# Optimization experiments

Hardware: AMD Instinct MI355X
Metric: run time of the kernel (lower is better)

The kernel has to match this reference:

```python
import jax, jax.numpy as jnp
import numpy as np

N0, P1 = 10000, 30000
N1 = N0 + P1            # 40000
P2 = 120000
N2 = N1 + P2            # 160000
E0, E1, E2 = 60000, 120000, 480000
IN, H, OUT, K = 3, 192, 3, 2


def setup_inputs() -> dict:
    key = jax.random.key(0)
    k = jax.random.split(key, 13)
    return {
        "features": jax.random.normal(k[0], (N0, IN), jnp.float32),
        "src0": jax.random.randint(k[1], (E0,), 0, N0, jnp.int32),
        "dst0": jax.random.randint(k[2], (E0,), 0, N0, jnp.int32),
        "pool_idx0": jax.random.randint(k[3], (P1, 2), 0, N0, jnp.int32),
        "edge0": jax.random.randint(k[4], (E1, 2), 0, N1, jnp.int32),
        "pool_idx1": jax.random.randint(k[5], (P2, 2), 0, N1, jnp.int32),
        "edge1": jax.random.randint(k[6], (E2, 2), 0, N2, jnp.int32),
        "W_first": 0.3 * jax.random.normal(k[7], (3, (K + 1) * IN, H), jnp.float32),
        "b_first": jnp.zeros((3, H), jnp.float32),
        "W_mid": 0.04 * jax.random.normal(k[8], (3, 12, (K + 1) * H, H), jnp.float32),
        "b_mid": jnp.zeros((3, 12, H), jnp.float32),
        "W_last": 0.05 * jax.random.normal(k[9], (3, (K + 1) * H, OUT), jnp.float32),
        "b_last": jnp.zeros((3, OUT), jnp.float32),
    }


def _norm(dst, n):
    # symmetric-norm factor D^{-1/2}, degrees clamped at 1 (DGL TAGConv)
    deg = jax.ops.segment_sum(jnp.ones(dst.shape[0], jnp.float32), dst, num_segments=n)
    return jnp.clip(deg, 1.0) ** -0.5  # [n]


def _tagconv(x, src, dst, n, norm, W, b):
    fs = [x]
    h = x
    for _ in range(K):
        h = norm[:, None] * jax.ops.segment_sum((h * norm[:, None])[src], dst, num_segments=n)
        fs.append(h)
    return jnp.concatenate(fs, axis=1) @ W + b


def _stage(x, src, dst, n, Wf, bf, Wm, bm, Wl, bl):
    norm = _norm(dst, n)
    h = jax.nn.relu(_tagconv(x, src, dst, n, norm, Wf, bf))
    prev = h  # raw output of previous layer (hidden[-2] in the torch code)
    for i in range(12):
        cur = jax.nn.relu(_tagconv(h, src, dst, n, norm, Wm[i], bm[i]))
        h = 0.5 * (prev + cur) if (i + 1) in (2, 4, 6, 8, 10, 12) else cur
        prev = cur
    return _tagconv(h, src, dst, n, norm, Wl, bl)  # identity activation


def _unpool(feat, pool_idx):
    # new vertex = midpoint of its two parents; appended to the node table
    new_vs = 0.5 * (feat[pool_idx[:, 0]] + feat[pool_idx[:, 1]])
    return jnp.concatenate([feat, new_vs], axis=0)


def _bidir(edge):
    # graph.add_edges(src, dst); graph.add_edges(dst, src)
    return (jnp.concatenate([edge[:, 0], edge[:, 1]]),
            jnp.concatenate([edge[:, 1], edge[:, 0]]))


def reference(features, src0, dst0, pool_idx0, edge0, pool_idx1, edge1,
              W_first, b_first, W_mid, b_mid, W_last, b_last):
    out1 = _stage(features, src0, dst0, N0,
                  W_first[0], b_first[0], W_mid[0], b_mid[0], W_last[0], b_last[0])
    h = _unpool(out1, pool_idx0)            # [N1, 3]
    out1_2 = h
    s1, d1 = _bidir(edge0)
    out2 = _stage(h, s1, d1, N1,
                  W_first[1], b_first[1], W_mid[1], b_mid[1], W_last[1], b_last[1])
    h = _unpool(out2, pool_idx1)            # [N2, 3]
    out2_2 = h
    s2, d2 = _bidir(edge1)
    out3 = _stage(h, s2, d2, N2,
                  W_first[2], b_first[2], W_mid[2], b_mid[2], W_last[2], b_last[2])
    return (out1, out2, out3, out1_2, out2_2)
```

## Files before the change

### kernel.cpp

```cpp
#include <hip/hip_runtime.h>
#include <hip/hip_fp16.h>

#define HF 192

static inline int divup(int a, int b){ return (a+b-1)/b; }

typedef _Float16 half8 __attribute__((ext_vector_type(8)));
typedef float f32x4 __attribute__((ext_vector_type(4)));

#define G_WS_BYTES 195734272ull
__device__ __align__(256) char g_ws[G_WS_BYTES];

#define OFF_HH    0ull
#define OFF_T1H   61440000ull
#define OFF_T2H   122880000ull
#define OFF_DEG  184320000ull
#define OFF_RP   184960000ull
#define OFF_COL  185600032ull
#define OFF_NRM  189440032ull
#define OFF_O1F  190080032ull
#define OFF_U1F  190200032ull
#define OFF_O2F  190680032ull
#define OFF_U2F  191160032ull
#define OFF_WT   193080032ull
#define OFF_X1F  OFF_T1H
#define OFF_X2F  (OFF_T1H + 1920000ull)

__device__ __forceinline__ float*  wsf(unsigned long long o){ return (float*) (g_ws + o); }
__device__ __forceinline__ int*    wsi(unsigned long long o){ return (int*)   (g_ws + o); }
__device__ __forceinline__ __half* wsh(unsigned long long o){ return (__half*)(g_ws + o); }

__global__ void k_zero(unsigned long long off, int n) {
  int i = blockIdx.x*blockDim.x + threadIdx.x;
  if (i < n) wsi(off)[i] = 0;
}
__global__ void k_copyi(unsigned long long aOff, unsigned long long bOff, int n) {
  int i = blockIdx.x*blockDim.x + threadIdx.x;
  if (i < n) wsi(bOff)[i] = wsi(aOff)[i];
}

__global__ void k_count_direct(const int* __restrict__ dst, int E) {
  int* deg = wsi(OFF_DEG);
  int e = blockIdx.x*blockDim.x + threadIdx.x;
  if (e < E) atomicAdd(&deg[dst[e]], 1);
}
__global__ void k_count_bidir(const int* __restrict__ edge, int E) {
  int* deg = wsi(OFF_DEG);
  int e = blockIdx.x*blockDim.x + threadIdx.x;
  if (e < E) {
    atomicAdd(&deg[edge[2*e+1]], 1);
    atomicAdd(&deg[edge[2*e  ]], 1);
  }
}
__global__ void k_norm(int n) {
  const int* deg = wsi(OFF_DEG);
  float* nrm = wsf(OFF_NRM);
  int i = blockIdx.x*blockDim.x + threadIdx.x;
  if (i < n) {
    int d = deg[i]; if (d < 1) d = 1;
    nrm[i] = rsqrtf((float)d);
  }
}
__global__ __launch_bounds__(1024) void k_exscan(int n) {
  const int* in = wsi(OFF_DEG);
  int* out = wsi(OFF_RP);
  __shared__ int sm[1024];
  int t = threadIdx.x;
  int carry = 0;
  for (int base = 0; base < n; base += 4096) {
    int idx = base + t*4;
    int v0 = (idx+0 < n) ? in[idx+0] : 0;
    int v1 = (idx+1 < n) ? in[idx+1] : 0;
    int v2 = (idx+2 < n) ? in[idx+2] : 0;
    int v3 = (idx+3 < n) ? in[idx+3] : 0;
    int s = v0+v1+v2+v3;
    sm[t] = s;
    __syncthreads();
    for (int off = 1; off < 1024; off <<= 1) {
      int u = (t >= off) ? sm[t-off] : 0;
      __syncthreads();
      sm[t] += u;
      __syncthreads();
    }
    int excl = carry + sm[t] - s;
    if (idx   < n) out[idx]   = excl;
    if (idx+1 < n) out[idx+1] = excl + v0;
    if (idx+2 < n) out[idx+2] = excl + v0+v1;
    if (idx+3 < n) out[idx+3] = excl + v0+v1+v2;
    carry += sm[1023];
    __syncthreads();
  }
  if (t == 0) out[n] = carry;
}
__global__ void k_fill_direct(const int* __restrict__ src, const int* __restrict__ dst, int E) {
  int* cur = wsi(OFF_DEG);
  int* col = wsi(OFF_COL);
  int e = blockIdx.x*blockDim.x + threadIdx.x;
  if (e < E) {
    int p = atomicAdd(&cur[dst[e]], 1);
    col[p] = src[e];
  }
}
__global__ void k_fill_bidir(const int* __restrict__ edge, int E) {
  int* cur = wsi(OFF_DEG);
  int* col = wsi(OFF_COL);
  int e = blockIdx.x*blockDim.x + threadIdx.x;
  if (e < E) {
    int u = edge[2*e], v = edge[2*e+1];
    int p = atomicAdd(&cur[v], 1); col[p] = u;
    int q = atomicAdd(&cur[u], 1); col[q] = v;
  }
}

__global__ void k_spmm3(const float* __restrict__ Xext, unsigned long long Xoff,
                        unsigned long long Yoff, int n) {
  const float* X = Xext ? Xext : wsf(Xoff);
  float* Y = wsf(Yoff);
  const int* rowptr = wsi(OFF_RP);
  const int* col = wsi(OFF_COL);
  const float* nrm = wsf(OFF_NRM);
  int row = blockIdx.x*blockDim.x + threadIdx.x;
  if (row >= n) return;
  int s = rowptr[row], e = rowptr[row+1];
  float a0=0.f, a1=0.f, a2=0.f;
  for (int i = s; i < e; ++i) {
    int c = col[i]; float v = nrm[c];
    a0 = fmaf(v, X[c*3+0], a0);
    a1 = fmaf(v, X[c*3+1], a1);
    a2 = fmaf(v, X[c*3+2], a2);
  }
  float nm = nrm[row];
  Y[row*3+0] = a0*nm; Y[row*3+1] = a1*nm; Y[row*3+2] = a2*nm;
}

__global__ __launch_bounds__(192) void k_spmm8(unsigned long long Xoff,
                                               unsigned long long Yoff, int n) {
  int gid = blockIdx.x*192 + threadIdx.x;
  if (gid >= n*24) return;
  int row = gid / 24, f8 = gid - row*24;
  const half8* __restrict__ X8 = (const half8*)wsh(Xoff);
  half8* __restrict__ Y8 = (half8*)wsh(Yoff);
  const int* rowptr = wsi(OFF_RP);
  const int* col = wsi(OFF_COL);
  const float* nrm = wsf(OFF_NRM);
  int s = rowptr[row], e = rowptr[row+1];
  float acc[8];
  #pragma unroll
  for (int j = 0; j < 8; ++j) acc[j] = 0.f;
  for (int i = s; i < e; ++i) {
    int c = col[i];
    float w = nrm[c];
    half8 v = X8[(size_t)c*24 + f8];
    #pragma unroll
    for (int j = 0; j < 8; ++j) acc[j] = fmaf(w, (float)v[j], acc[j]);
  }
  float nm = nrm[row];
  half8 r;
  #pragma unroll
  for (int j = 0; j < 8; ++j) r[j] = (_Float16)(acc[j]*nm);
  Y8[(size_t)row*24 + f8] = r;
}

__global__ void k_gemm_first(const float* __restrict__ xext, unsigned long long xOff,
                             const float* __restrict__ W, const float* __restrict__ b, int n) {
  const float* x  = xext ? xext : wsf(xOff);
  const float* x1 = wsf(OFF_X1F);
  const float* x2 = wsf(OFF_X2F);
  __half* H = wsh(OFF_HH);
  int idx = blockIdx.x*blockDim.x + threadIdx.x;
  if (idx >= n*HF) return;
  int row = idx / HF, c = idx - row*HF;
  float acc = b[c];
  #pragma unroll
  for (int k = 0; k < 3; ++k) acc = fmaf(x [row*3+k], W[(0+k)*HF + c], acc);
  #pragma unroll
  for (int k = 0; k < 3; ++k) acc = fmaf(x1[row*3+k], W[(3+k)*HF + c], acc);
  #pragma unroll
  for (int k = 0; k < 3; ++k) acc = fmaf(x2[row*3+k], W[(6+k)*HF + c], acc);
  H[idx] = __float2half(fmaxf(acc, 0.f));
}

__global__ void k_wprep(const float* __restrict__ Wm, int s) {
  int idx = blockIdx.x*blockDim.x + threadIdx.x;
  if (idx >= 12*576*HF) return;
  int it = idx / (576*HF);
  int rem = idx - it*576*HF;
  int k = rem / HF;
  int c = rem - k*HF;
  wsh(OFF_WT)[(size_t)it*HF*576 + (size_t)c*576 + k] =
      __float2half(Wm[((size_t)(s*12+it)*576 + k)*HF + c]);
}

#define BPAD 104
__global__ __launch_bounds__(256) void k_mfma_mid(
    const float* __restrict__ b, int it, int n, int residual)
{
  __half* __restrict__ H = wsh(OFF_HH);
  const __half* __restrict__ T1 = wsh(OFF_T1H);
  const __half* __restrict__ T2 = wsh(OFF_T2H);
  const __half* __restrict__ Wt = wsh(OFF_WT) + (size_t)it*HF*576;
  __shared__ _Float16 Bs[192*BPAD];
  int t = threadIdx.x;
  int w = t >> 6;
  int l = t & 63;
  int lr = l & 15;
  int lg = l >> 4;
  int row0 = blockIdx.x*64 + w*16;

  f32x4 acc[12];
  #pragma unroll
  for (int i = 0; i < 12; ++i) acc[i] = (f32x4){0.f,0.f,0.f,0.f};

  const __half* Xp[3] = { H, T1, T2 };
  for (int p = 0; p < 3; ++p) {
    const __half* X = Xp[p];
    for (int kh = 0; kh < 2; ++kh) {
      __syncthreads();
      for (int i = t; i < 192*12; i += 256) {
        int c  = i / 12;
        int k8 = i - c*12;
        *(half8*)&Bs[c*BPAD + k8*8] =
            *(const half8*)&Wt[(size_t)c*576 + p*HF + kh*96 + k8*8];
      }
      __syncthreads();
      #pragma unroll
      for (int k0 = 0; k0 < 96; k0 += 32) {
        half8 a = *(const half8*)&X[(size_t)(row0 + lr)*HF + kh*96 + k0 + lg*8];
        #pragma unroll
        for (int tl = 0; tl < 12; ++tl) {
          half8 bb = *(const half8*)&Bs[(tl*16 + lr)*BPAD + k0 + lg*8];
          acc[tl] = __builtin_amdgcn_mfma_f32_16x16x32_f16(a, bb, acc[tl], 0, 0, 0);
        }
      }
    }
  }

  #pragma unroll
  for (int tl = 0; tl < 12; ++tl) {
    int c = tl*16 + lr;
    float bias = b[c];
    #pragma unroll
    for (int j = 0; j < 4; ++j) {
      int row = row0 + lg*4 + j;
      if (row < n) {
        size_t o = (size_t)row*HF + c;
        float cur = fmaxf(acc[tl][j] + bias, 0.f);
        float h = cur;
        if (residual) h = 0.5f*(__half2float(H[o]) + cur);
        H[o] = __float2half(h);
      }
    }
  }
}

__global__ void k_last_lin(const float* __restrict__ W, const float* __restrict__ b,
                           float* __restrict__ outb, unsigned long long outfOff,
                           int hasOutf, int n) {
  int row = blockIdx.x*blockDim.x + threadIdx.x;
  if (row >= n) return;
  const __half* H  = wsh(OFF_HH);
  const __half* T1 = wsh(OFF_T1H);
  const __half* T2 = wsh(OFF_T2H);
  float a0 = b[0], a1 = b[1], a2 = b[2];
  const __half* x = &H[(size_t)row*HF];
  for (int k = 0; k < HF; ++k) {
    float v = __half2float(x[k]); const float* w = &W[k*3];
    a0 = fmaf(v, w[0], a0); a1 = fmaf(v, w[1], a1); a2 = fmaf(v, w[2], a2);
  }
  x = &T1[(size_t)row*HF];
  for (int k = 0; k < HF; ++k) {
    float v = __half2float(x[k]); const float* w = &W[(HF+k)*3];
    a0 = fmaf(v, w[0], a0); a1 = fmaf(v, w[1], a1); a2 = fmaf(v, w[2], a2);
  }
  x = &T2[(size_t)row*HF];
  for (int k = 0; k < HF; ++k) {
    float v = __half2float(x[k]); const float* w = &W[(2*HF+k)*3];
    a0 = fmaf(v, w[0], a0); a1 = fmaf(v, w[1], a1); a2 = fmaf(v, w[2], a2);
  }
  outb[row*3+0] = a0;
  outb[row*3+1] = a1;
  outb[row*3+2] = a2;
  if (hasOutf) {
    float* outf = wsf(outfOff);
    outf[row*3+0] = a0; outf[row*3+1] = a1; outf[row*3+2] = a2;
  }
}

__global__ void k_unpool(unsigned long long srcOff, const int* __restrict__ pidx,
                         unsigned long long dstfOff, float* __restrict__ dstb,
                         int n, int P) {
  const float* src = wsf(srcOff);
  float* dstf = wsf(dstfOff);
  int i = blockIdx.x*blockDim.x + threadIdx.x;
  if (i >= n + P) return;
  float v0, v1, v2;
  if (i < n) {
    v0 = src[i*3+0]; v1 = src[i*3+1]; v2 = src[i*3+2];
  } else {
    int a = pidx[(i-n)*2], c = pidx[(i-n)*2+1];
    v0 = 0.5f*(src[a*3+0] + src[c*3+0]);
    v1 = 0.5f*(src[a*3+1] + src[c*3+1]);
    v2 = 0.5f*(src[a*3+2] + src[c*3+2]);
  }
  dstf[i*3+0] = v0; dstf[i*3+1] = v1; dstf[i*3+2] = v2;
  dstb[i*3+0] = v0;
  dstb[i*3+1] = v1;
  dstb[i*3+2] = v2;
}

extern "C" void kernel_launch(void* const* d_in, const int* in_sizes, int n_in,
                              void* d_out, int out_size, void* d_ws, size_t ws_size,
                              hipStream_t stream) {
  (void)in_sizes; (void)n_in; (void)out_size; (void)d_ws; (void)ws_size;
  const float* features = (const float*)d_in[0];
  const int*  src0  = (const int*)d_in[1];
  const int*  dst0  = (const int*)d_in[2];
  const int*  pool0 = (const int*)d_in[3];
  const int*  edge0 = (const int*)d_in[4];
  const int*  pool1 = (const int*)d_in[5];
  const int*  edge1 = (const int*)d_in[6];
  const float* Wf = (const float*)d_in[7];
  const float* bfp = (const float*)d_in[8];
  const float* Wm = (const float*)d_in[9];
  const float* bm = (const float*)d_in[10];
  const float* Wl = (const float*)d_in[11];
  const float* bl = (const float*)d_in[12];
  float* out = (float*)d_out;

  auto csr = [&](int n, const int* srcD, const int* dstD, int Edir,
                 const int* edgeB, int Eund) {
    k_zero<<<divup(n,256),256,0,stream>>>(OFF_DEG, n);
    if (srcD) k_count_direct<<<divup(Edir,256),256,0,stream>>>(dstD, Edir);
    else      k_count_bidir <<<divup(Eund,256),256,0,stream>>>(edgeB, Eund);
    k_norm<<<divup(n,256),256,0,stream>>>(n);
    k_exscan<<<1,1024,0,stream>>>(n);
    k_copyi<<<divup(n,256),256,0,stream>>>(OFF_RP, OFF_DEG, n);
    if (srcD) k_fill_direct<<<divup(Edir,256),256,0,stream>>>(srcD, dstD, Edir);
    else      k_fill_bidir <<<divup(Eund,256),256,0,stream>>>(edgeB, Eund);
  };

  auto stage_u = [&](const float* xext, unsigned long long xOff, int n,
                     const int* srcD, const int* dstD, int Edir,
                     const int* edgeB, int Eund,
                     int s, float* outb, unsigned long long outfOff, int hasOutf) {
    csr(n, srcD, dstD, Edir, edgeB, Eund);
    k_wprep<<<divup(12*576*HF,256),256,0,stream>>>(Wm, s);
    k_spmm3<<<divup(n,256),256,0,stream>>>(xext, xOff, OFF_X1F, n);
    k_spmm3<<<divup(n,256),256,0,stream>>>(nullptr, OFF_X1F, OFF_X2F, n);
    k_gemm_first<<<divup(n*HF,256),256,0,stream>>>(xext, xOff,
        Wf + (size_t)s*9*HF, bfp + s*HF, n);
    int gsp = divup(n*24,192);
    for (int it = 0; it < 12; ++it) {
      k_spmm8<<<gsp,192,0,stream>>>(OFF_HH,  OFF_T1H, n);
      k_spmm8<<<gsp,192,0,stream>>>(OFF_T1H, OFF_T2H, n);
      k_mfma_mid<<<divup(n,64),256,0,stream>>>(bm + (s*12+it)*HF, it, n,
          ((it+1)%2==0) ? 1 : 0);
    }
    k_spmm8<<<gsp,192,0,stream>>>(OFF_HH,  OFF_T1H, n);
    k_spmm8<<<gsp,192,0,stream>>>(OFF_T1H, OFF_T2H, n);
    k_last_lin<<<divup(n,256),256,0,stream>>>(Wl + (size_t)s*576*3, bl + s*3,
        outb, outfOff, hasOutf, n);
  };

  stage_u(features, 0ull, 10000, src0, dst0, 60000, nullptr, 0,
          0, out + 0, OFF_O1F, 1);
  k_unpool<<<divup(40000,256),256,0,stream>>>(OFF_O1F, pool0, OFF_U1F, out + 630000, 10000, 30000);
  stage_u(nullptr, OFF_U1F, 40000, nullptr, nullptr, 0, edge0, 120000,
          1, out + 30000, OFF_O2F, 1);
  k_unpool<<<divup(160000,256),256,0,stream>>>(OFF_O2F, pool1, OFF_U2F, out + 750000, 40000, 120000);
  stage_u(nullptr, OFF_U2F, 160000, nullptr, nullptr, 0, edge1, 480000,
          2, out + 150000, OFF_O1F, 0);
}
```

Measured before the change: 5.937 ms.

## Double MFMA row tile, unroll SpMM gather by two, vectorize last linear

The mid-layer MFMA kernel now computes 32 rows per wave instead of 16, so each B tile staged in LDS is reused across twice as many rows and per-row weight staging is halved. It also carries a min-blocks launch bound. The SpMM kernel processes two neighbors per iteration with separate accumulators to expose more memory-level parallelism. The last linear layer reads features as half8 vectors. Risks are higher register pressure from 24 accumulators and fewer blocks for small graphs. Rows past n are still read unguarded in the A loads, as before.

Result: no change. 6.055 ms (+2.0%).

```diff
diff --git a/kernel.cpp b/kernel.cpp
--- a/kernel.cpp
+++ b/kernel.cpp
@@ -144,20 +144,32 @@
   const int* col = wsi(OFF_COL);
   const float* nrm = wsf(OFF_NRM);
   int s = rowptr[row], e = rowptr[row+1];
-  float acc[8];
-  #pragma unroll
-  for (int j = 0; j < 8; ++j) acc[j] = 0.f;
-  for (int i = s; i < e; ++i) {
-    int c = col[i];
-    float w = nrm[c];
-    half8 v = X8[(size_t)c*24 + f8];
+  float acc0[8], acc1[8];
+  #pragma unroll
+  for (int j = 0; j < 8; ++j) { acc0[j] = 0.f; acc1[j] = 0.f; }
+  int i = s;
+  for (; i + 2 <= e; i += 2) {
+    int c0 = col[i], c1 = col[i+1];
+    float w0 = nrm[c0], w1 = nrm[c1];
+    half8 v0 = X8[(size_t)c0*24 + f8];
+    half8 v1 = X8[(size_t)c1*24 + f8];
     #pragma unroll
-    for (int j = 0; j < 8; ++j) acc[j] = fmaf(w, (float)v[j], acc[j]);
+    for (int j = 0; j < 8; ++j) {
+      acc0[j] = fmaf(w0, (float)v0[j], acc0[j]);
+      acc1[j] = fmaf(w1, (float)v1[j], acc1[j]);
+    }
+  }
+  if (i < e) {
+    int c0 = col[i];
+    float w0 = nrm[c0];
+    half8 v0 = X8[(size_t)c0*24 + f8];
+    #pragma unroll
+    for (int j = 0; j < 8; ++j) acc0[j] = fmaf(w0, (float)v0[j], acc0[j]);
   }
   float nm = nrm[row];
   half8 r;
   #pragma unroll
-  for (int j = 0; j < 8; ++j) r[j] = (_Float16)(acc[j]*nm);
+  for (int j = 0; j < 8; ++j) r[j] = (_Float16)((acc0[j] + acc1[j])*nm);
   Y8[(size_t)row*24 + f8] = r;
 }
 
@@ -192,7 +204,7 @@
 }
 
 #define BPAD 104
-__global__ __launch_bounds__(256) void k_mfma_mid(
+__global__ __launch_bounds__(256,4) void k_mfma_mid(
     const float* __restrict__ b, int it, int n, int residual)
 {
   __half* __restrict__ H = wsh(OFF_HH);
@@ -205,11 +217,13 @@
   int l = t & 63;
   int lr = l & 15;
   int lg = l >> 4;
-  int row0 = blockIdx.x*64 + w*16;
-
-  f32x4 acc[12];
-  #pragma unroll
-  for (int i = 0; i < 12; ++i) acc[i] = (f32x4){0.f,0.f,0.f,0.f};
+  int row0 = blockIdx.x*128 + w*32;
+
+  f32x4 acc[2][12];
+  #pragma unroll
+  for (int s2 = 0; s2 < 2; ++s2)
+    #pragma unroll
+    for (int i = 0; i < 12; ++i) acc[s2][i] = (f32x4){0.f,0.f,0.f,0.f};
 
   const __half* Xp[3] = { H, T1, T2 };
   for (int p = 0; p < 3; ++p) {
@@ -225,29 +239,34 @@
       __syncthreads();
       #pragma unroll
       for (int k0 = 0; k0 < 96; k0 += 32) {
-        half8 a = *(const half8*)&X[(size_t)(row0 + lr)*HF + kh*96 + k0 + lg*8];
+        half8 a0 = *(const half8*)&X[(size_t)(row0 + lr     )*HF + kh*96 + k0 + lg*8];
+        half8 a1 = *(const half8*)&X[(size_t)(row0 + 16 + lr)*HF + kh*96 + k0 + lg*8];
         #pragma unroll
         for (int tl = 0; tl < 12; ++tl) {
           half8 bb = *(const half8*)&Bs[(tl*16 + lr)*BPAD + k0 + lg*8];
-          acc[tl] = __builtin_amdgcn_mfma_f32_16x16x32_f16(a, bb, acc[tl], 0, 0, 0);
+          acc[0][tl] = __builtin_amdgcn_mfma_f32_16x16x32_f16(a0, bb, acc[0][tl], 0, 0, 0);
+          acc[1][tl] = __builtin_amdgcn_mfma_f32_16x16x32_f16(a1, bb, acc[1][tl], 0, 0, 0);
         }
       }
     }
   }
 
   #pragma unroll
-  for (int tl = 0; tl < 12; ++tl) {
-    int c = tl*16 + lr;
-    float bias = b[c];
+  for (int s2 = 0; s2 < 2; ++s2) {
     #pragma unroll
-    for (int j = 0; j < 4; ++j) {
-      int row = row0 + lg*4 + j;
-      if (row < n) {
-        size_t o = (size_t)row*HF + c;
-        float cur = fmaxf(acc[tl][j] + bias, 0.f);
-        float h = cur;
-        if (residual) h = 0.5f*(__half2float(H[o]) + cur);
-        H[o] = __float2half(h);
+    for (int tl = 0; tl < 12; ++tl) {
+      int c = tl*16 + lr;
+      float bias = b[c];
+      #pragma unroll
+      for (int j = 0; j < 4; ++j) {
+        int row = row0 + s2*16 + lg*4 + j;
+        if (row < n) {
+          size_t o = (size_t)row*HF + c;
+          float cur = fmaxf(acc[s2][tl][j] + bias, 0.f);
+          float h = cur;
+          if (residual) h = 0.5f*(__half2float(H[o]) + cur);
+          H[o] = __float2half(h);
+        }
       }
     }
   }
@@ -258,24 +277,21 @@
                            int hasOutf, int n) {
   int row = blockIdx.x*blockDim.x + threadIdx.x;
   if (row >= n) return;
-  const __half* H  = wsh(OFF_HH);
-  const __half* T1 = wsh(OFF_T1H);
-  const __half* T2 = wsh(OFF_T2H);
+  const __half* bufs[3] = { wsh(OFF_HH), wsh(OFF_T1H), wsh(OFF_T2H) };
   float a0 = b[0], a1 = b[1], a2 = b[2];
-  const __half* x = &H[(size_t)row*HF];
-  for (int k = 0; k < HF; ++k) {
-    float v = __half2float(x[k]); const float* w = &W[k*3];
-    a0 = fmaf(v, w[0], a0); a1 = fmaf(v, w[1], a1); a2 = fmaf(v, w[2], a2);
-  }
-  x = &T1[(size_t)row*HF];
-  for (int k = 0; k < HF; ++k) {
-    float v = __half2float(x[k]); const float* w = &W[(HF+k)*3];
-    a0 = fmaf(v, w[0], a0); a1 = fmaf(v, w[1], a1); a2 = fmaf(v, w[2], a2);
-  }
-  x = &T2[(size_t)row*HF];
-  for (int k = 0; k < HF; ++k) {
-    float v = __half2float(x[k]); const float* w = &W[(2*HF+k)*3];
-    a0 = fmaf(v, w[0], a0); a1 = fmaf(v, w[1], a1); a2 = fmaf(v, w[2], a2);
+  for (int p = 0; p < 3; ++p) {
+    const half8* x8 = (const half8*)&bufs[p][(size_t)row*HF];
+    #pragma unroll 4
+    for (int k8 = 0; k8 < 24; ++k8) {
+      half8 v = x8[k8];
+      #pragma unroll
+      for (int j = 0; j < 8; ++j) {
+        int k = k8*8 + j;
+        const float* w = &W[(p*HF + k)*3];
+        float vv = (float)v[j];
+        a0 = fmaf(vv, w[0], a0); a1 = fmaf(vv, w[1], a1); a2 = fmaf(vv, w[2], a2);
+      }
+    }
   }
   outb[row*3+0] = a0;
   outb[row*3+1] = a1;
@@ -353,7 +369,7 @@
     for (int it = 0; it < 12; ++it) {
       k_spmm8<<<gsp,192,0,stream>>>(OFF_HH,  OFF_T1H, n);
       k_spmm8<<<gsp,192,0,stream>>>(OFF_T1H, OFF_T2H, n);
-      k_mfma_mid<<<divup(n,64),256,0,stream>>>(bm + (s*12+it)*HF, it, n,
+      k_mfma_mid<<<divup(n,128),256,0,stream>>>(bm + (s*12+it)*HF, it, n,
           ((it+1)%2==0) ? 1 : 0);
     }
     k_spmm8<<<gsp,192,0,stream>>>(OFF_HH,  OFF_T1H, n);
```
